# Kernel optimization log

Hardware: AMD Instinct MI355X
Metric: run time of the kernel (lower is better)

Reference implementation:

```python
import jax, jax.numpy as jnp
import numpy as np

B, C, H, W, K, NH = 4, 128, 64, 64, 7, 8
DH = C // NH          # per-head dim
PAD = (K - 1) // 2    # symmetric padding since K is odd


def setup_inputs() -> dict:
    key = jax.random.key(0)
    ks = jax.random.split(key, 9)
    s = 1.0 / np.sqrt(C)
    f32 = jnp.float32
    return {
        "x": jax.random.normal(ks[0], (B, C, H, W), f32),
        "wq": jax.random.normal(ks[1], (C, C), f32) * s,
        "bq": jax.random.normal(ks[2], (C,), f32) * 0.01,
        "wk": jax.random.normal(ks[3], (C, C), f32) * s,
        "bk": jax.random.normal(ks[4], (C,), f32) * 0.01,
        "wv": jax.random.normal(ks[5], (C, C), f32) * s,
        "bv": jax.random.normal(ks[6], (C,), f32) * 0.01,
        "pos_h": jax.random.normal(ks[7], (NH, K), f32) * 0.02,
        "pos_w": jax.random.normal(ks[8], (NH, K), f32) * 0.02,
    }


def _unfold(p):
    # p: [B,C,H+K-1,W+K-1] -> [B,C,H,W,K,K] (KxK neighborhood per pixel),
    # matching torch .unfold(2,K,1).unfold(3,K,1). Loop is over fixed kernel size only.
    p1 = jnp.stack([p[:, :, i:i + H, :] for i in range(K)], axis=-1)      # [B,C,H,W+K-1,K]
    return jnp.stack([p1[:, :, :, j:j + W, :] for j in range(K)], axis=-1)  # [B,C,H,W,K,K]


def reference(x, wq, bq, wk, bk, wv, bv, pos_h, pos_w):
    cx = x  # cx defaults to x in the original module
    pc = jnp.pad(cx, ((0, 0), (0, 0), (PAD, PAD), (PAD, PAD)))
    # 1x1 convs are pointwise channel mixes
    k = jnp.einsum('oc,bchw->bohw', wk, pc) + bk[None, :, None, None]
    v = jnp.einsum('oc,bchw->bohw', wv, pc) + bv[None, :, None, None]
    q = jnp.einsum('oc,bchw->bohw', wq, x) + bq[None, :, None, None]

    ku = _unfold(k).reshape(B, NH, DH, H, W, K, K)
    vu = _unfold(v).reshape(B, NH, DH, H, W, K, K)
    qh = q.reshape(B, NH, DH, H, W)

    # per-pixel logits over KxK neighborhood
    logits = jnp.einsum('bndhw,bndhwij->bnhwij', qh, ku)  # [B,NH,H,W,K,K]
    logits = logits + pos_h[None, :, None, None, :, None] + pos_w[None, :, None, None, None, :]

    weights = jax.nn.softmax(logits.reshape(B, NH, H, W, K * K), axis=-1)
    out = jnp.einsum('bnhwk,bndhwk->bndhw', weights, vu.reshape(B, NH, DH, H, W, K * K))
    return out.reshape(B, C, H, W)
```

## Files before the change

kernel.cpp:

```cpp
#include <hip/hip_runtime.h>
#include <cmath>

constexpr int Bn = 4, Cn = 128, Hn = 64, Wn = 64, Kn = 7, NHn = 8, DHn = 16, PADn = 3;
constexpr int HWn = Hn * Wn;
constexpr int TS = 16;
constexpr size_t QPLANE = (size_t)Bn * NHn * HWn * DHn;

constexpr int SP   = 64;
constexpr int XROW = 136;

constexpr int HR = 22;
constexpr int HC = 24;
constexpr int KP = 24;
constexpr int VW = 14;

typedef float f32x4 __attribute__((ext_vector_type(4)));
typedef short short8 __attribute__((ext_vector_type(8)));
typedef unsigned int u32x4 __attribute__((ext_vector_type(4)));
typedef unsigned short u16x4 __attribute__((ext_vector_type(4)));
typedef unsigned short u16x8 __attribute__((ext_vector_type(8)));

__device__ __forceinline__ unsigned short f32_to_bf16_rne(float f) {
  unsigned u = __float_as_uint(f);
  unsigned r = u + 0x7fffu + ((u >> 16) & 1u);
  return (unsigned short)(r >> 16);
}
__device__ __forceinline__ float bf16_to_f32(unsigned short h) {
  return __uint_as_float(((unsigned)h) << 16);
}
__device__ __forceinline__ unsigned pk_bf16(float lo, float hi) {
  return (__float_as_uint(lo) >> 16) | (__float_as_uint(hi) & 0xffff0000u);
}
__device__ __forceinline__ f32x4 max4(f32x4 a, f32x4 b) {
  a[0] = fmaxf(a[0], b[0]); a[1] = fmaxf(a[1], b[1]);
  a[2] = fmaxf(a[2], b[2]); a[3] = fmaxf(a[3], b[3]);
  return a;
}

union UVcast { u32x4 u; short8 s; };

__global__ __launch_bounds__(512)
void qkv_fused(const float* __restrict__ x,
               const float* __restrict__ wq, const float* __restrict__ wk,
               const float* __restrict__ wv,
               const float* __restrict__ bq_, const float* __restrict__ bk_,
               const float* __restrict__ bv_,
               unsigned short* __restrict__ qo, unsigned short* __restrict__ kbf,
               unsigned short* __restrict__ vbf)
{
  __shared__ float smf[32][SP + 1];
  __shared__ __align__(16) unsigned short xthi[SP * XROW];
  __shared__ __align__(16) unsigned short xtlo[SP * XROW];

  const int b   = blockIdx.z;
  const int p0  = blockIdx.x * SP;
  const int tid = threadIdx.x;
  const float* xb = x + (size_t)b * Cn * HWn;

  f32x4 xr0, xr1, xr2, xr3;
  {
    const int c  = tid >> 4;
    const int p4 = (tid & 15) * 4;
    const float* bp = xb + (size_t)c * HWn + p0 + p4;
    xr0 = *reinterpret_cast<const f32x4*>(bp);
    xr1 = *reinterpret_cast<const f32x4*>(bp + (size_t)32 * HWn);
    xr2 = *reinterpret_cast<const f32x4*>(bp + (size_t)64 * HWn);
    xr3 = *reinterpret_cast<const f32x4*>(bp + (size_t)96 * HWn);
  }

#pragma unroll
  for (int cc = 0; cc < 4; ++cc) {
    const f32x4 v = (cc == 0) ? xr0 : (cc == 1) ? xr1 : (cc == 2) ? xr2 : xr3;
    const int cl = tid >> 4;
    const int p4 = (tid & 15) * 4;
    smf[cl][p4 + 0] = v[0]; smf[cl][p4 + 1] = v[1];
    smf[cl][p4 + 2] = v[2]; smf[cl][p4 + 3] = v[3];
    __syncthreads();
    if (tid < 256) {
      const int pl  = tid >> 2;
      const int c0l = (tid & 3) * 8;
      u32x4 hw, lw;
#pragma unroll
      for (int j = 0; j < 4; ++j) {
        const float v0 = smf[c0l + 2 * j][pl];
        const float v1 = smf[c0l + 2 * j + 1][pl];
        const unsigned short h0 = f32_to_bf16_rne(v0);
        const unsigned short h1 = f32_to_bf16_rne(v1);
        const unsigned short l0 = f32_to_bf16_rne(v0 - bf16_to_f32(h0));
        const unsigned short l1 = f32_to_bf16_rne(v1 - bf16_to_f32(h1));
        hw[j] = h0 | ((unsigned)h1 << 16);
        lw[j] = l0 | ((unsigned)l1 << 16);
      }
      const int csw = (cc * 32 + c0l) ^ ((pl & 7) << 3);
      *reinterpret_cast<u32x4*>(xthi + pl * XROW + csw) = hw;
      *reinterpret_cast<u32x4*>(xtlo + pl * XROW + csw) = lw;
    }
    __syncthreads();
  }

  const int wave = tid >> 6;
  if (wave >= 6) return;
  const int lane = tid & 63;
  const int r    = lane & 15;
  const int quad = lane >> 4;
  const int mat  = wave >> 1;
  const int half = wave & 1;
  const int mbase = half * 64;
  const float* Wsel = (mat == 0) ? wq : (mat == 1) ? wk : wv;
  const float* bias = (mat == 0) ? bq_ : (mat == 1) ? bk_ : bv_;

  f32x4 acc[4][4] = {};

#pragma unroll
  for (int ks = 0; ks < 4; ++ks) {
    const int kk = ks * 32 + quad * 8;
    short8 Ah[4], Al[4], Bh[4], Bl[4];
#pragma unroll
    for (int mt = 0; mt < 4; ++mt) {
      const float* wp = Wsel + (size_t)(mbase + mt * 16 + r) * Cn + kk;
      const f32x4 wa = *reinterpret_cast<const f32x4*>(wp);
      const f32x4 wb = *reinterpret_cast<const f32x4*>(wp + 4);
      short8 ah, al;
#pragma unroll
      for (int j = 0; j < 4; ++j) {
        const unsigned short h = f32_to_bf16_rne(wa[j]);
        ah[j] = (short)h;
        al[j] = (short)f32_to_bf16_rne(wa[j] - bf16_to_f32(h));
      }
#pragma unroll
      for (int j = 0; j < 4; ++j) {
        const unsigned short h = f32_to_bf16_rne(wb[j]);
        ah[4 + j] = (short)h;
        al[4 + j] = (short)f32_to_bf16_rne(wb[j] - bf16_to_f32(h));
      }
      Ah[mt] = ah; Al[mt] = al;
    }
#pragma unroll
    for (int nt = 0; nt < 4; ++nt) {
      const int px  = nt * 16 + r;
      const int csw = kk ^ ((px & 7) << 3);
      Bh[nt] = *reinterpret_cast<const short8*>(xthi + px * XROW + csw);
      Bl[nt] = *reinterpret_cast<const short8*>(xtlo + px * XROW + csw);
    }
#pragma unroll
    for (int mt = 0; mt < 4; ++mt)
#pragma unroll
      for (int nt = 0; nt < 4; ++nt) {
        acc[mt][nt] = __builtin_amdgcn_mfma_f32_16x16x32_bf16(Ah[mt], Bh[nt], acc[mt][nt], 0, 0, 0);
        acc[mt][nt] = __builtin_amdgcn_mfma_f32_16x16x32_bf16(Ah[mt], Bl[nt], acc[mt][nt], 0, 0, 0);
        acc[mt][nt] = __builtin_amdgcn_mfma_f32_16x16x32_bf16(Al[mt], Bh[nt], acc[mt][nt], 0, 0, 0);
      }
  }

#pragma unroll
  for (int mt = 0; mt < 4; ++mt) {
    const int n = half * 4 + mt;
    const f32x4 b4 = *reinterpret_cast<const f32x4*>(bias + mbase + mt * 16 + quad * 4);
#pragma unroll
    for (int nt = 0; nt < 4; ++nt) {
      const int p = p0 + nt * 16 + r;
      const size_t off = ((size_t)((b * NHn + n) * HWn + p)) * DHn + quad * 4;
      f32x4 val = acc[mt][nt] + b4;
      if (mat == 0) {
        u16x4 hi4, lo4;
#pragma unroll
        for (int j = 0; j < 4; ++j) {
          const unsigned short hb = f32_to_bf16_rne(val[j]);
          hi4[j] = hb;
          lo4[j] = f32_to_bf16_rne(val[j] - bf16_to_f32(hb));
        }
        *reinterpret_cast<u16x4*>(qo + off)          = hi4;
        *reinterpret_cast<u16x4*>(qo + QPLANE + off) = lo4;
      } else {
        unsigned short* y = (mat == 1) ? kbf : vbf;
        u16x4 pkv;
        pkv[0] = f32_to_bf16_rne(val[0]); pkv[1] = f32_to_bf16_rne(val[1]);
        pkv[2] = f32_to_bf16_rne(val[2]); pkv[3] = f32_to_bf16_rne(val[3]);
        *reinterpret_cast<u16x4*>(y + off) = pkv;
      }
    }
  }
}

__global__ __launch_bounds__(256)
void sasa_attn(const unsigned short* __restrict__ qhl,
               const unsigned short* __restrict__ kbf,
               const unsigned short* __restrict__ vbf,
               const float* __restrict__ bk_, const float* __restrict__ bv_,
               const float* __restrict__ pos_h, const float* __restrict__ pos_w,
               float* __restrict__ out)
{
  __shared__ __align__(16) unsigned short ksm[HR * HC * KP];
  __shared__ __align__(16) unsigned       vsm[HR * DHn * VW];

  const int z  = blockIdx.z;
  const int b  = z >> 3;
  const int n  = z & 7;
  const int h0 = blockIdx.y * TS;
  const int w0 = blockIdx.x * TS;
  const int tid  = threadIdx.x;
  const int lane = tid & 63;
  const int wv   = tid >> 6;
  const int r    = lane & 15;
  const int quad = lane >> 4;
  const int cbase = n * DHn;

  const unsigned short* kb = kbf + ((size_t)(b * NHn + n) * HWn) * DHn;
  const unsigned short* vb = vbf + ((size_t)(b * NHn + n) * HWn) * DHn;
  const size_t qbase = ((size_t)(b * NHn + n) * HWn) * DHn;
  const unsigned short* qhp = qhl + qbase;
  const unsigned short* qlp = qhl + QPLANE + qbase;

  u16x8 kb0, kb1, vb0, vb1;
#pragma unroll
  for (int j = 0; j < 8; ++j) {
    kb0[j] = f32_to_bf16_rne(bk_[cbase + j]);
    kb1[j] = f32_to_bf16_rne(bk_[cbase + 8 + j]);
    vb0[j] = f32_to_bf16_rne(bv_[cbase + j]);
    vb1[j] = f32_to_bf16_rne(bv_[cbase + 8 + j]);
  }

  for (int c = tid; c < HR * HC * 2; c += 256) {
    const int pix  = c >> 1;
    const int half = c & 1;
    const int hh = pix / HC;
    const int ww = pix - hh * HC;
    const int gh = h0 + hh - PADn;
    const int gw = w0 + ww - PADn;
    const bool inb = (gh >= 0) && (gh < Hn) && (gw >= 0) && (gw < Wn);
    u16x8 kd;
    if (inb) kd = *reinterpret_cast<const u16x8*>(kb + ((size_t)(gh * Wn + gw)) * DHn + half * 8);
    else     kd = half ? kb1 : kb0;
    *reinterpret_cast<u16x8*>(ksm + pix * KP + half * 8) = kd;
  }

  for (int pp = tid; pp < HR * (HC / 2); pp += 256) {
    const int hh = pp / (HC / 2);
    const int wp = pp - hh * (HC / 2);
    const int gh = h0 + hh - PADn;
    u16x8 a0, a1, c0, c1;
    {
      const int gw = w0 + 2 * wp - PADn;
      const bool inb = (gh >= 0) && (gh < Hn) && (gw >= 0) && (gw < Wn);
      if (inb) {
        const size_t src = ((size_t)(gh * Wn + gw)) * DHn;
        a0 = *reinterpret_cast<const u16x8*>(vb + src);
        a1 = *reinterpret_cast<const u16x8*>(vb + src + 8);
      } else { a0 = vb0; a1 = vb1; }
    }
    {
      const int gw = w0 + 2 * wp + 1 - PADn;
      const bool inb = (gh >= 0) && (gh < Hn) && (gw >= 0) && (gw < Wn);
      if (inb) {
        const size_t src = ((size_t)(gh * Wn + gw)) * DHn;
        c0 = *reinterpret_cast<const u16x8*>(vb + src);
        c1 = *reinterpret_cast<const u16x8*>(vb + src + 8);
      } else { c0 = vb0; c1 = vb1; }
    }
    unsigned* dst = vsm + (hh * DHn) * VW + wp;
#pragma unroll
    for (int d = 0; d < 8; ++d)
      dst[d * VW] = (unsigned)(unsigned short)a0[d] | ((unsigned)(unsigned short)c0[d] << 16);
#pragma unroll
    for (int d = 0; d < 8; ++d)
      dst[(8 + d) * VW] = (unsigned)(unsigned short)a1[d] | ((unsigned)(unsigned short)c1[d] << 16);
  }

  float ph[7];
#pragma unroll
  for (int i = 0; i < 7; ++i) ph[i] = pos_h[n * Kn + i];
  f32x4 pw4[2];
#pragma unroll
  for (int win = 0; win < 2; ++win) {
#pragma unroll
    for (int reg = 0; reg < 4; ++reg) {
      const int ww = win * 8 + 4 * quad + reg;
      const int j  = ww - r;
      const bool valid = (j >= 0) && (j < 7) && (win == 0 || ww >= 16);
      const int jc = j < 0 ? 0 : (j > 6 ? 6 : j);
      const float pv = pos_w[n * Kn + jc];
      pw4[win][reg] = valid ? pv : -1e30f;
    }
  }

  __syncthreads();

  const f32x4 zero4 = {};
  for (int hl = 0; hl < 4; ++hl) {
    const int h = wv * 4 + hl;

    const int pix = (h0 + h) * Wn + (w0 + r);
    const unsigned short* qsel = (quad < 2) ? qhp : qlp;
    const short8 qf = *reinterpret_cast<const short8*>(qsel + (size_t)pix * DHn + (quad & 1) * 8);

    f32x4 L[14];
#pragma unroll
    for (int i = 0; i < 7; ++i) {
#pragma unroll
      for (int win = 0; win < 2; ++win) {
        const short8 kf = *reinterpret_cast<const short8*>(
            ksm + ((h + i) * HC + win * 8 + r) * KP + (quad & 1) * 8);
        f32x4 d = __builtin_amdgcn_mfma_f32_16x16x32_bf16(kf, qf, zero4, 0, 0, 0);
        d = d + pw4[win];
        d = d + (f32x4)ph[i];
        L[i * 2 + win] = d;
      }
    }

    f32x4 M4 = L[0];
#pragma unroll
    for (int t = 1; t < 14; ++t) M4 = max4(M4, L[t]);
    float m = fmaxf(fmaxf(M4[0], M4[1]), fmaxf(M4[2], M4[3]));
    m = fmaxf(m, __shfl_xor(m, 16, 64));
    m = fmaxf(m, __shfl_xor(m, 32, 64));

    f32x4 S4 = {};
#pragma unroll
    for (int t = 0; t < 14; ++t) {
      f32x4 e;
      e[0] = __expf(L[t][0] - m);
      e[1] = __expf(L[t][1] - m);
      e[2] = __expf(L[t][2] - m);
      e[3] = __expf(L[t][3] - m);
      L[t] = e;
      S4 += e;
    }
    float s = (S4[0] + S4[1]) + (S4[2] + S4[3]);
    s += __shfl_xor(s, 16, 64);
    s += __shfl_xor(s, 32, 64);
    const float inv = 1.0f / s;

    f32x4 oA = {}, oB = {};
#pragma unroll
    for (int i = 0; i < 7; ++i) {
      const f32x4 e0 = L[2 * i]     * (f32x4)inv;
      const f32x4 e1 = L[2 * i + 1] * (f32x4)inv;
      UVcast A;
      A.u[0] = pk_bf16(e0[0], e0[1]);
      A.u[1] = pk_bf16(e0[2], e0[3]);
      A.u[2] = pk_bf16(e1[0], e1[1]);
      A.u[3] = pk_bf16(e1[2], e1[3]);

      const unsigned* vp = vsm + ((h + i) * DHn + r) * VW + 2 * quad;
      const uint2 v0 = *reinterpret_cast<const uint2*>(vp);
      const uint2 v1 = *reinterpret_cast<const uint2*>(vp + 4);
      UVcast Bv;
      Bv.u[0] = v0.x; Bv.u[1] = v0.y; Bv.u[2] = v1.x; Bv.u[3] = v1.y;

      f32x4& acc = (i & 1) ? oB : oA;
      acc = __builtin_amdgcn_mfma_f32_16x16x32_bf16(A.s, Bv.s, acc, 0, 0, 0);
    }
    const f32x4 O = oA + oB;

    float* op = out + ((size_t)(b * Cn + cbase + r)) * HWn + (h0 + h) * Wn + w0 + 4 * quad;
    *reinterpret_cast<f32x4*>(op) = O;
  }
}

extern "C" void kernel_launch(void* const* d_in, const int* in_sizes, int n_in,
                              void* d_out, int out_size, void* d_ws, size_t ws_size,
                              hipStream_t stream) {
  const float* x     = (const float*)d_in[0];
  const float* wq    = (const float*)d_in[1];
  const float* bq    = (const float*)d_in[2];
  const float* wk    = (const float*)d_in[3];
  const float* bk    = (const float*)d_in[4];
  const float* wv    = (const float*)d_in[5];
  const float* bv    = (const float*)d_in[6];
  const float* pos_h = (const float*)d_in[7];
  const float* pos_w = (const float*)d_in[8];
  float* out = (float*)d_out;

  const size_t tensor_elems = (size_t)Bn * Cn * HWn;
  unsigned short* qhl = (unsigned short*)d_ws;
  unsigned short* kbf = qhl + 2 * tensor_elems;
  unsigned short* vbf = kbf + tensor_elems;

  dim3 gq(HWn / SP, 1, Bn);
  qkv_fused<<<gq, 512, 0, stream>>>(x, wq, wk, wv, bq, bk, bv, qhl, kbf, vbf);

  dim3 g2(Wn / TS, Hn / TS, Bn * NHn);
  sasa_attn<<<g2, 256, 0, stream>>>(qhl, kbf, vbf, bk, bv, pos_h, pos_w, out);
}
```

Before: 107.0 us.

## Batch x staging, remap attention blocks per XCD, prefetch Q, pad V smem

The qkv kernel now stages all four channel chunks into a larger shared buffer with a single barrier, and all 512 threads do the bf16 hi/lo split in two passes. Before, eight barriers were needed and only half the threads converted. The attention kernel remaps its flat block index so that the 16 tiles of one (batch, head) land on the same XCD, aiming for better L2 reuse of K/V halos. It also preloads all four Q fragments before the main loop, and pads the V shared-memory row from 14 to 15 to reduce bank conflicts. In exchange, shared memory use and register pressure both rise.

New measurement: 120.7 us. +12.8%, slower.

```diff
diff --git a/kernel.cpp b/kernel.cpp
--- a/kernel.cpp
+++ b/kernel.cpp
@@ -12,7 +12,7 @@
 constexpr int HR = 22;
 constexpr int HC = 24;
 constexpr int KP = 24;
-constexpr int VW = 14;
+constexpr int VW = 15;
 
 typedef float f32x4 __attribute__((ext_vector_type(4)));
 typedef short short8 __attribute__((ext_vector_type(8)));
@@ -48,7 +48,7 @@
                unsigned short* __restrict__ qo, unsigned short* __restrict__ kbf,
                unsigned short* __restrict__ vbf)
 {
-  __shared__ float smf[32][SP + 1];
+  __shared__ float smf[4][32][SP + 1];
   __shared__ __align__(16) unsigned short xthi[SP * XROW];
   __shared__ __align__(16) unsigned short xtlo[SP * XROW];
 
@@ -68,35 +68,44 @@
     xr3 = *reinterpret_cast<const f32x4*>(bp + (size_t)96 * HWn);
   }
 
-#pragma unroll
-  for (int cc = 0; cc < 4; ++cc) {
-    const f32x4 v = (cc == 0) ? xr0 : (cc == 1) ? xr1 : (cc == 2) ? xr2 : xr3;
+  {
     const int cl = tid >> 4;
     const int p4 = (tid & 15) * 4;
-    smf[cl][p4 + 0] = v[0]; smf[cl][p4 + 1] = v[1];
-    smf[cl][p4 + 2] = v[2]; smf[cl][p4 + 3] = v[3];
-    __syncthreads();
-    if (tid < 256) {
-      const int pl  = tid >> 2;
-      const int c0l = (tid & 3) * 8;
-      u32x4 hw, lw;
-#pragma unroll
-      for (int j = 0; j < 4; ++j) {
-        const float v0 = smf[c0l + 2 * j][pl];
-        const float v1 = smf[c0l + 2 * j + 1][pl];
-        const unsigned short h0 = f32_to_bf16_rne(v0);
-        const unsigned short h1 = f32_to_bf16_rne(v1);
-        const unsigned short l0 = f32_to_bf16_rne(v0 - bf16_to_f32(h0));
-        const unsigned short l1 = f32_to_bf16_rne(v1 - bf16_to_f32(h1));
-        hw[j] = h0 | ((unsigned)h1 << 16);
-        lw[j] = l0 | ((unsigned)l1 << 16);
-      }
-      const int csw = (cc * 32 + c0l) ^ ((pl & 7) << 3);
-      *reinterpret_cast<u32x4*>(xthi + pl * XROW + csw) = hw;
-      *reinterpret_cast<u32x4*>(xtlo + pl * XROW + csw) = lw;
-    }
-    __syncthreads();
-  }
+#pragma unroll
+    for (int j = 0; j < 4; ++j) smf[0][cl][p4 + j] = xr0[j];
+#pragma unroll
+    for (int j = 0; j < 4; ++j) smf[1][cl][p4 + j] = xr1[j];
+#pragma unroll
+    for (int j = 0; j < 4; ++j) smf[2][cl][p4 + j] = xr2[j];
+#pragma unroll
+    for (int j = 0; j < 4; ++j) smf[3][cl][p4 + j] = xr3[j];
+  }
+  __syncthreads();
+
+#pragma unroll
+  for (int rep = 0; rep < 2; ++rep) {
+    const int task = rep * 512 + tid;
+    const int cc   = task >> 8;
+    const int t2   = task & 255;
+    const int pl   = t2 >> 2;
+    const int c0l  = (t2 & 3) * 8;
+    u32x4 hw, lw;
+#pragma unroll
+    for (int j = 0; j < 4; ++j) {
+      const float v0 = smf[cc][c0l + 2 * j][pl];
+      const float v1 = smf[cc][c0l + 2 * j + 1][pl];
+      const unsigned short h0 = f32_to_bf16_rne(v0);
+      const unsigned short h1 = f32_to_bf16_rne(v1);
+      const unsigned short l0 = f32_to_bf16_rne(v0 - bf16_to_f32(h0));
+      const unsigned short l1 = f32_to_bf16_rne(v1 - bf16_to_f32(h1));
+      hw[j] = h0 | ((unsigned)h1 << 16);
+      lw[j] = l0 | ((unsigned)l1 << 16);
+    }
+    const int csw = (cc * 32 + c0l) ^ ((pl & 7) << 3);
+    *reinterpret_cast<u32x4*>(xthi + pl * XROW + csw) = hw;
+    *reinterpret_cast<u32x4*>(xtlo + pl * XROW + csw) = lw;
+  }
+  __syncthreads();
 
   const int wave = tid >> 6;
   if (wave >= 6) return;
@@ -193,11 +202,16 @@
   __shared__ __align__(16) unsigned short ksm[HR * HC * KP];
   __shared__ __align__(16) unsigned       vsm[HR * DHn * VW];
 
-  const int z  = blockIdx.z;
+  const int flat = blockIdx.z * 16 + blockIdx.y * 4 + blockIdx.x;
+  const int xcd  = flat & 7;
+  const int slot = flat >> 3;
+  const int z    = xcd * 4 + (slot >> 4);
+  const int tile = slot & 15;
+
   const int b  = z >> 3;
   const int n  = z & 7;
-  const int h0 = blockIdx.y * TS;
-  const int w0 = blockIdx.x * TS;
+  const int h0 = (tile >> 2) * TS;
+  const int w0 = (tile & 3) * TS;
   const int tid  = threadIdx.x;
   const int lane = tid & 63;
   const int wv   = tid >> 6;
@@ -210,6 +224,14 @@
   const size_t qbase = ((size_t)(b * NHn + n) * HWn) * DHn;
   const unsigned short* qhp = qhl + qbase;
   const unsigned short* qlp = qhl + QPLANE + qbase;
+
+  const unsigned short* qsel = (quad < 2) ? qhp : qlp;
+  short8 qf[4];
+#pragma unroll
+  for (int hl = 0; hl < 4; ++hl) {
+    const int pix = (h0 + wv * 4 + hl) * Wn + (w0 + r);
+    qf[hl] = *reinterpret_cast<const short8*>(qsel + (size_t)pix * DHn + (quad & 1) * 8);
+  }
 
   u16x8 kb0, kb1, vb0, vb1;
 #pragma unroll
@@ -289,10 +311,6 @@
   for (int hl = 0; hl < 4; ++hl) {
     const int h = wv * 4 + hl;
 
-    const int pix = (h0 + h) * Wn + (w0 + r);
-    const unsigned short* qsel = (quad < 2) ? qhp : qlp;
-    const short8 qf = *reinterpret_cast<const short8*>(qsel + (size_t)pix * DHn + (quad & 1) * 8);
-
     f32x4 L[14];
 #pragma unroll
     for (int i = 0; i < 7; ++i) {
@@ -300,7 +318,7 @@
       for (int win = 0; win < 2; ++win) {
         const short8 kf = *reinterpret_cast<const short8*>(
             ksm + ((h + i) * HC + win * 8 + r) * KP + (quad & 1) * 8);
-        f32x4 d = __builtin_amdgcn_mfma_f32_16x16x32_bf16(kf, qf, zero4, 0, 0, 0);
+        f32x4 d = __builtin_amdgcn_mfma_f32_16x16x32_bf16(kf, qf[hl], zero4, 0, 0, 0);
         d = d + pw4[win];
         d = d + (f32x4)ph[i];
         L[i * 2 + win] = d;
```
